# Performance work log

Hardware: AMD Instinct MI355X
Metric: run time of the kernel (lower is better)

## Reference

```python
import jax, jax.numpy as jnp
import numpy as np

N_NODES = 100000
N_EDGES = 1600000
D_IN = 128
HIDDEN = 64
N_CLASSES = 10
N_GRAPHS = 512


def setup_inputs() -> dict:
    key = jax.random.key(0)
    ks = jax.random.split(key, 9)
    x = jax.random.normal(ks[0], (N_NODES, D_IN), dtype=jnp.float32)
    edge_index = jax.random.randint(ks[1], (2, N_EDGES), 0, N_NODES, dtype=jnp.int32)
    batch = jnp.sort(jax.random.randint(ks[2], (N_NODES,), 0, N_GRAPHS, dtype=jnp.int32))
    # GCNConv: lin (no bias) + separate bias added after aggregation
    s1 = 1.0 / np.sqrt(D_IN)
    s2 = 1.0 / np.sqrt(HIDDEN)
    W1 = jax.random.uniform(ks[3], (D_IN, HIDDEN), jnp.float32, -s1, s1)
    b1 = jnp.zeros((HIDDEN,), jnp.float32)
    W2 = jax.random.uniform(ks[4], (HIDDEN, HIDDEN), jnp.float32, -s2, s2)
    b2 = jnp.zeros((HIDDEN,), jnp.float32)
    Wfc = jax.random.uniform(ks[5], (HIDDEN, N_CLASSES), jnp.float32, -s2, s2)
    bfc = jax.random.uniform(ks[6], (N_CLASSES,), jnp.float32, -s2, s2)
    return {"x": x, "edge_index": edge_index, "batch": batch,
            "W1": W1, "b1": b1, "W2": W2, "b2": b2, "Wfc": Wfc, "bfc": bfc}


def gcn_conv(x, src, dst, W, b, n_nodes):
    # symmetric normalization with added self-loops (PyG gcn_norm defaults)
    deg = jnp.zeros((n_nodes,), x.dtype).at[dst].add(1.0) + 1.0  # +1 self-loop
    dinv = jax.lax.rsqrt(deg)
    h = x @ W  # [N, out]
    coef = (dinv[src] * dinv[dst])[:, None]          # [E, 1]
    msg = h[src] * coef                               # [E, out]
    agg = jax.ops.segment_sum(msg, dst, num_segments=n_nodes)
    agg = agg + h * (dinv * dinv)[:, None]            # self-loop contribution
    return agg + b


def reference(x, edge_index, batch, W1, b1, W2, b2, Wfc, bfc):
    src, dst = edge_index[0], edge_index[1]
    n_nodes = x.shape[0]
    h = gcn_conv(x, src, dst, W1, b1, n_nodes)
    h = jax.nn.relu(h)
    # dropout skipped (inference, training=False)
    h = gcn_conv(h, src, dst, W2, b2, n_nodes)
    h = jax.nn.relu(h)
    # global mean pool over graphs
    sums = jax.ops.segment_sum(h, batch, num_segments=N_GRAPHS)
    cnts = jax.ops.segment_sum(jnp.ones((n_nodes,), h.dtype), batch, num_segments=N_GRAPHS)
    pooled = sums / jnp.maximum(cnts, 1.0)[:, None]   # [G, hidden]
    logits = pooled @ Wfc + bfc                        # [G, classes]
    return jax.nn.log_softmax(logits, axis=1)
```

## Files before the change

### kernel.cpp

```cpp
#include <hip/hip_runtime.h>
#include <cstdint>
#include <cstddef>

#define N_NODES   100000
#define N_EDGES   1600000
#define D_IN      128
#define HIDDEN    64
#define N_GRAPHS  512
#define N_CLASSES 10

#define NB   196
#define EB   1563
#define EB4  391
#define NBE  (NB * EB)
#define BCAP 12288
#define PSLOTS 8

typedef __attribute__((ext_vector_type(8))) short bf16x8;
typedef __attribute__((ext_vector_type(4))) float f32x4;
typedef __attribute__((ext_vector_type(2))) float f32x2;

__device__ inline float bf2f(unsigned short u) {
    return __uint_as_float(((unsigned int)u) << 16);
}
__device__ inline unsigned short f2bf(float f) {
    unsigned int x = __float_as_uint(f);
    return (unsigned short)((x + 0x7FFF + ((x >> 16) & 1)) >> 16);
}

__global__ __launch_bounds__(256)
void scan1_kernel(const int* __restrict__ in, int* __restrict__ bsum, int n) {
    __shared__ int lds[256];
    int tid = threadIdx.x;
    int base = blockIdx.x * 4096 + tid * 16;
    int s = 0;
#pragma unroll
    for (int j = 0; j < 16; j++) { int i = base + j; if (i < n) s += in[i]; }
    lds[tid] = s; __syncthreads();
    for (int off = 128; off > 0; off >>= 1) {
        if (tid < off) lds[tid] += lds[tid + off];
        __syncthreads();
    }
    if (tid == 0) bsum[blockIdx.x] = lds[0];
}

__global__ __launch_bounds__(256)
void scan2_kernel(int* __restrict__ bsum, int* __restrict__ out, int nb, int n) {
    __shared__ int lds[256];
    int tid = threadIdx.x;
    int v = (tid < nb) ? bsum[tid] : 0;
    lds[tid] = v; __syncthreads();
    for (int off = 1; off < 256; off <<= 1) {
        int t = (tid >= off) ? lds[tid - off] : 0;
        __syncthreads();
        lds[tid] += t;
        __syncthreads();
    }
    if (tid < nb) bsum[tid] = lds[tid] - v;
    if (tid == 255) out[n] = lds[255];
}

__global__ __launch_bounds__(256)
void scan3_kernel(const int* __restrict__ in, const int* __restrict__ bsum,
                  int* __restrict__ out, int n) {
    __shared__ int lds[256];
    int tid = threadIdx.x;
    int base = blockIdx.x * 4096 + tid * 16;
    int v[16]; int s = 0;
#pragma unroll
    for (int j = 0; j < 16; j++) {
        int i = base + j;
        v[j] = (i < n) ? in[i] : 0;
        s += v[j];
    }
    lds[tid] = s; __syncthreads();
    for (int off = 1; off < 256; off <<= 1) {
        int t = (tid >= off) ? lds[tid - off] : 0;
        __syncthreads();
        lds[tid] += t;
        __syncthreads();
    }
    int ex = lds[tid] - s + bsum[blockIdx.x];
#pragma unroll
    for (int j = 0; j < 16; j++) {
        int i = base + j;
        if (i < n) { out[i] = ex; ex += v[j]; }
    }
}

__global__ __launch_bounds__(256)
void fused1_kernel(const float* __restrict__ X, const float* __restrict__ W,
                   unsigned short* __restrict__ H,
                   const int* __restrict__ dst, int* __restrict__ HA) {
    const int tid = threadIdx.x;
    if (blockIdx.x & 1) {
        __shared__ int cnt[NB];
        int hb = blockIdx.x >> 1;
        for (int i = tid; i < NB; i += 256) cnt[i] = 0;
        __syncthreads();
        int base = hb * 1024 + tid;
#pragma unroll
        for (int j = 0; j < 4; j++) {
            int t = base + j * 256;
            if (t < N_EDGES) atomicAdd(&cnt[dst[t] >> 9], 1);
        }
        __syncthreads();
        for (int b = tid; b < NB; b += 256) HA[b * EB + hb] = cnt[b];
        return;
    }

    constexpr int K  = D_IN;
    constexpr int KP = K + 8;
    __shared__ unsigned short As[64 * KP];
    __shared__ unsigned short Wt[64 * KP];

    const int row0 = (blockIdx.x >> 1) * 64;

    for (int i = tid; i < K * 64; i += 256) {
        int k = i >> 6;
        int n = i & 63;
        Wt[n * KP + k] = f2bf(W[i]);
    }
    constexpr int KQ = K / 4;
    for (int i = tid; i < 64 * KQ; i += 256) {
        int r = i / KQ, k4 = i % KQ;
        int row = row0 + r;
        float4 v = make_float4(0.f, 0.f, 0.f, 0.f);
        if (row < N_NODES) v = ((const float4*)(X + (size_t)row * K))[k4];
        ushort4 o = make_ushort4(f2bf(v.x), f2bf(v.y), f2bf(v.z), f2bf(v.w));
        *(ushort4*)&As[r * KP + k4 * 4] = o;
    }
    __syncthreads();

    const int wave = tid >> 6;
    const int lane = tid & 63;
    const int lrow = lane & 15;
    const int quad = lane >> 4;
    const int m = wave * 16 + lrow;

    f32x4 acc0 = {0.f, 0.f, 0.f, 0.f};
    f32x4 acc1 = {0.f, 0.f, 0.f, 0.f};
    f32x4 acc2 = {0.f, 0.f, 0.f, 0.f};
    f32x4 acc3 = {0.f, 0.f, 0.f, 0.f};

#pragma unroll
    for (int kt = 0; kt < K / 32; kt++) {
        int k0 = kt * 32 + quad * 8;
        bf16x8 a = *(const bf16x8*)&As[m * KP + k0];
        bf16x8 b0 = *(const bf16x8*)&Wt[(0 * 16 + lrow) * KP + k0];
        bf16x8 b1 = *(const bf16x8*)&Wt[(1 * 16 + lrow) * KP + k0];
        bf16x8 b2 = *(const bf16x8*)&Wt[(2 * 16 + lrow) * KP + k0];
        bf16x8 b3 = *(const bf16x8*)&Wt[(3 * 16 + lrow) * KP + k0];
        acc0 = __builtin_amdgcn_mfma_f32_16x16x32_bf16(a, b0, acc0, 0, 0, 0);
        acc1 = __builtin_amdgcn_mfma_f32_16x16x32_bf16(a, b1, acc1, 0, 0, 0);
        acc2 = __builtin_amdgcn_mfma_f32_16x16x32_bf16(a, b2, acc2, 0, 0, 0);
        acc3 = __builtin_amdgcn_mfma_f32_16x16x32_bf16(a, b3, acc3, 0, 0, 0);
    }

    f32x4 accs[4] = {acc0, acc1, acc2, acc3};
#pragma unroll
    for (int c = 0; c < 4; c++) {
#pragma unroll
        for (int r = 0; r < 4; r++) {
            int row = row0 + wave * 16 + quad * 4 + r;
            if (row < N_NODES) H[(size_t)row * 64 + c * 16 + lrow] = f2bf(accs[c][r]);
        }
    }
}

__global__ __launch_bounds__(256)
void scatterA2_kernel(const int* __restrict__ src, const int* __restrict__ dst,
                      const int* __restrict__ posA, int2* __restrict__ edgeA) {
    __shared__ int off[NB];
    int tid = threadIdx.x, blk = blockIdx.x;
    for (int b = tid; b < NB; b += 256) off[b] = posA[b * EB + blk * 4];
    __syncthreads();
    int base = blk * 4096 + tid;
#pragma unroll
    for (int j = 0; j < 16; j++) {
        int t = base + j * 256;
        if (t < N_EDGES) {
            int d = dst[t];
            int r = atomicAdd(&off[d >> 9], 1);
            edgeA[r] = make_int2(d, src[t]);
        }
    }
}

__global__ __launch_bounds__(256)
void passB_kernel(const int* __restrict__ posA, const int2* __restrict__ edgeA,
                  int* __restrict__ noffs, float* __restrict__ dinv,
                  int* __restrict__ srcs2) {
    __shared__ int hist[512];
    __shared__ int off[512];
    __shared__ int ps[256];
    __shared__ int srcs_l[BCAP];

    int tid = threadIdx.x, b = blockIdx.x;
    int e0 = posA[b * EB];
    int e1 = posA[(b + 1) * EB];
    int n0 = b << 9;
    int nn = min(512, N_NODES - n0);
    int len = e1 - e0;

    hist[tid] = 0; hist[tid + 256] = 0;
    __syncthreads();
    for (int i = e0 + tid; i < e1; i += 256) atomicAdd(&hist[edgeA[i].x - n0], 1);
    __syncthreads();

    for (int n = tid; n < nn; n += 256) dinv[n0 + n] = rsqrtf((float)hist[n] + 1.0f);

    int a0 = hist[2 * tid], a1 = hist[2 * tid + 1];
    ps[tid] = a0 + a1;
    __syncthreads();
    for (int d = 1; d < 256; d <<= 1) {
        int v = (tid >= d) ? ps[tid - d] : 0;
        __syncthreads();
        ps[tid] += v;
        __syncthreads();
    }
    int pre = ps[tid] - (a0 + a1);
    off[2 * tid] = pre;
    off[2 * tid + 1] = pre + a0;
    __syncthreads();

    for (int n = tid; n < nn; n += 256) noffs[n0 + n] = e0 + off[n];
    if (b == NB - 1 && tid == 0) noffs[N_NODES] = N_EDGES;
    __syncthreads();

    if (len <= BCAP) {
        for (int i = e0 + tid; i < e1; i += 256) {
            int2 e = edgeA[i];
            int r = atomicAdd(&off[e.x - n0], 1);
            srcs_l[r] = e.y;
        }
        __syncthreads();
        for (int i = tid; i < len; i += 256) srcs2[e0 + i] = srcs_l[i];
    } else {
        for (int i = e0 + tid; i < e1; i += 256) {
            int2 e = edgeA[i];
            int r = atomicAdd(&off[e.x - n0], 1);
            srcs2[e0 + r] = e.y;
        }
    }
}

template <int K>
__global__ __launch_bounds__(256)
void gemm_mfma_fp8out_kernel(const unsigned short* __restrict__ X, const float* __restrict__ W,
                             unsigned char* __restrict__ H8, int n_rows) {
    constexpr int KP = K + 8;
    __shared__ unsigned short As[64 * KP];
    __shared__ unsigned short Wt[64 * KP];

    const int tid  = threadIdx.x;
    const int row0 = blockIdx.x * 64;

    for (int i = tid; i < K * 64; i += 256) {
        int k = i >> 6;
        int n = i & 63;
        Wt[n * KP + k] = f2bf(W[i]);
    }
    constexpr int KQ = K / 8;
    for (int i = tid; i < 64 * KQ; i += 256) {
        int r = i / KQ, k8 = i % KQ;
        int row = row0 + r;
        int4 v = make_int4(0, 0, 0, 0);
        if (row < n_rows) v = ((const int4*)(X + (size_t)row * K))[k8];
        *(int4*)&As[r * KP + k8 * 8] = v;
    }
    __syncthreads();

    const int wave = tid >> 6;
    const int lane = tid & 63;
    const int lrow = lane & 15;
    const int quad = lane >> 4;
    const int m = wave * 16 + lrow;

    f32x4 acc0 = {0.f, 0.f, 0.f, 0.f};
    f32x4 acc1 = {0.f, 0.f, 0.f, 0.f};
    f32x4 acc2 = {0.f, 0.f, 0.f, 0.f};
    f32x4 acc3 = {0.f, 0.f, 0.f, 0.f};

#pragma unroll
    for (int kt = 0; kt < K / 32; kt++) {
        int k0 = kt * 32 + quad * 8;
        bf16x8 a = *(const bf16x8*)&As[m * KP + k0];
        bf16x8 b0 = *(const bf16x8*)&Wt[(0 * 16 + lrow) * KP + k0];
        bf16x8 b1 = *(const bf16x8*)&Wt[(1 * 16 + lrow) * KP + k0];
        bf16x8 b2 = *(const bf16x8*)&Wt[(2 * 16 + lrow) * KP + k0];
        bf16x8 b3 = *(const bf16x8*)&Wt[(3 * 16 + lrow) * KP + k0];
        acc0 = __builtin_amdgcn_mfma_f32_16x16x32_bf16(a, b0, acc0, 0, 0, 0);
        acc1 = __builtin_amdgcn_mfma_f32_16x16x32_bf16(a, b1, acc1, 0, 0, 0);
        acc2 = __builtin_amdgcn_mfma_f32_16x16x32_bf16(a, b2, acc2, 0, 0, 0);
        acc3 = __builtin_amdgcn_mfma_f32_16x16x32_bf16(a, b3, acc3, 0, 0, 0);
    }

    f32x4 accs[4] = {acc0, acc1, acc2, acc3};
#pragma unroll
    for (int c = 0; c < 4; c++) {
#pragma unroll
        for (int r = 0; r < 4; r++) {
            int row = row0 + wave * 16 + quad * 4 + r;
            if (row < n_rows) {
                int p = __builtin_amdgcn_cvt_pk_fp8_f32(accs[c][r], accs[c][r], 0, false);
                H8[(size_t)row * 64 + c * 16 + lrow] = (unsigned char)(p & 0xFF);
            }
        }
    }
}

__device__ inline void upk_fma(int4 u, float c, float* acc) {
    unsigned int a = (unsigned int)u.x, b = (unsigned int)u.y;
    unsigned int d = (unsigned int)u.z, e = (unsigned int)u.w;
    acc[0] += __uint_as_float(a << 16) * c;
    acc[1] += __uint_as_float(a & 0xFFFF0000u) * c;
    acc[2] += __uint_as_float(b << 16) * c;
    acc[3] += __uint_as_float(b & 0xFFFF0000u) * c;
    acc[4] += __uint_as_float(d << 16) * c;
    acc[5] += __uint_as_float(d & 0xFFFF0000u) * c;
    acc[6] += __uint_as_float(e << 16) * c;
    acc[7] += __uint_as_float(e & 0xFFFF0000u) * c;
}

__global__ __launch_bounds__(256)
void gather_flat_kernel(const int* __restrict__ offs, const int* __restrict__ srcs,
                        const float* __restrict__ dinv, const unsigned short* __restrict__ h,
                        const float* __restrict__ b, unsigned short* __restrict__ out,
                        int n_nodes) {
    int t = blockIdx.x * 256 + threadIdx.x;
    int node = t >> 3;
    if (node >= n_nodes) return;
    int cg = (t & 7) * 8;

    float dn = dinv[node];
    float acc[8];
    {
        int4 u = *(const int4*)(h + (size_t)node * 64 + cg);
        float c2 = dn * dn;
        for (int j = 0; j < 8; j++) acc[j] = 0.f;
        upk_fma(u, c2, acc);
    }

    int i  = offs[node];
    int i1 = offs[node + 1];
    for (; i + 4 <= i1; i += 4) {
        int s0 = srcs[i];
        int s1 = srcs[i + 1];
        int s2 = srcs[i + 2];
        int s3 = srcs[i + 3];
        float c0 = dinv[s0] * dn;
        float c1 = dinv[s1] * dn;
        float c2 = dinv[s2] * dn;
        float c3 = dinv[s3] * dn;
        int4 u0 = *(const int4*)(h + (size_t)s0 * 64 + cg);
        int4 u1 = *(const int4*)(h + (size_t)s1 * 64 + cg);
        int4 u2 = *(const int4*)(h + (size_t)s2 * 64 + cg);
        int4 u3 = *(const int4*)(h + (size_t)s3 * 64 + cg);
        upk_fma(u0, c0, acc);
        upk_fma(u1, c1, acc);
        upk_fma(u2, c2, acc);
        upk_fma(u3, c3, acc);
    }
    for (; i < i1; i++) {
        int s0 = srcs[i];
        float c0 = dinv[s0] * dn;
        int4 u0 = *(const int4*)(h + (size_t)s0 * 64 + cg);
        upk_fma(u0, c0, acc);
    }

    float4 b0 = *(const float4*)(b + cg);
    float4 b1 = *(const float4*)(b + cg + 4);
    unsigned short* o = out + (size_t)node * 64 + cg;
    ushort4 p0 = make_ushort4(f2bf(fmaxf(acc[0] + b0.x, 0.f)), f2bf(fmaxf(acc[1] + b0.y, 0.f)),
                              f2bf(fmaxf(acc[2] + b0.z, 0.f)), f2bf(fmaxf(acc[3] + b0.w, 0.f)));
    ushort4 p1 = make_ushort4(f2bf(fmaxf(acc[4] + b1.x, 0.f)), f2bf(fmaxf(acc[5] + b1.y, 0.f)),
                              f2bf(fmaxf(acc[6] + b1.z, 0.f)), f2bf(fmaxf(acc[7] + b1.w, 0.f)));
    *(ushort4*)(o)     = p0;
    *(ushort4*)(o + 4) = p1;
}

__device__ inline void upk8_fma(int2 u, float c, float* acc) {
    f32x2 p0 = __builtin_amdgcn_cvt_pk_f32_fp8(u.x, false);
    f32x2 p1 = __builtin_amdgcn_cvt_pk_f32_fp8(u.x, true);
    f32x2 p2 = __builtin_amdgcn_cvt_pk_f32_fp8(u.y, false);
    f32x2 p3 = __builtin_amdgcn_cvt_pk_f32_fp8(u.y, true);
    acc[0] += p0.x * c; acc[1] += p0.y * c;
    acc[2] += p1.x * c; acc[3] += p1.y * c;
    acc[4] += p2.x * c; acc[5] += p2.y * c;
    acc[6] += p3.x * c; acc[7] += p3.y * c;
}

__global__ __launch_bounds__(256)
void gather_fp8_pool_kernel(const int* __restrict__ offs, const int* __restrict__ srcs,
                            const float* __restrict__ dinv, const unsigned char* __restrict__ h8,
                            const float* __restrict__ b, const int* __restrict__ batch,
                            float* __restrict__ pooled, float* __restrict__ cnt,
                            int n_nodes) {
    __shared__ float pacc[PSLOTS][64];
    __shared__ float lcnt[PSLOTS];
    __shared__ int sg[2];

    int tid = threadIdx.x;
    int node0 = blockIdx.x * 32;
    int lastn = min(node0 + 31, n_nodes - 1);
    for (int i = tid; i < PSLOTS * 64; i += 256) ((float*)pacc)[i] = 0.f;
    if (tid < PSLOTS) lcnt[tid] = 0.f;
    if (tid == 0) { sg[0] = batch[min(node0, n_nodes - 1)]; sg[1] = batch[lastn]; }
    __syncthreads();
    int g0 = sg[0];
    bool single = (sg[0] == sg[1]);

    int node = node0 + (tid >> 3);
    int cg = (tid & 7) * 8;

    float r[8];
#pragma unroll
    for (int j = 0; j < 8; j++) r[j] = 0.f;

    if (node < n_nodes) {
        float dn = dinv[node];
        float acc[8];
        {
            int2 u = *(const int2*)(h8 + (size_t)node * 64 + cg);
            float c2 = dn * dn;
            for (int j = 0; j < 8; j++) acc[j] = 0.f;
            upk8_fma(u, c2, acc);
        }

        int i  = offs[node];
        int i1 = offs[node + 1];
        for (; i + 4 <= i1; i += 4) {
            int s0 = srcs[i];
            int s1 = srcs[i + 1];
            int s2 = srcs[i + 2];
            int s3 = srcs[i + 3];
            float c0 = dinv[s0] * dn;
            float c1 = dinv[s1] * dn;
            float c2 = dinv[s2] * dn;
            float c3 = dinv[s3] * dn;
            int2 u0 = *(const int2*)(h8 + (size_t)s0 * 64 + cg);
            int2 u1 = *(const int2*)(h8 + (size_t)s1 * 64 + cg);
            int2 u2 = *(const int2*)(h8 + (size_t)s2 * 64 + cg);
            int2 u3 = *(const int2*)(h8 + (size_t)s3 * 64 + cg);
            upk8_fma(u0, c0, acc);
            upk8_fma(u1, c1, acc);
            upk8_fma(u2, c2, acc);
            upk8_fma(u3, c3, acc);
        }
        for (; i < i1; i++) {
            int s0 = srcs[i];
            float c0 = dinv[s0] * dn;
            int2 u0 = *(const int2*)(h8 + (size_t)s0 * 64 + cg);
            upk8_fma(u0, c0, acc);
        }

        float4 b0 = *(const float4*)(b + cg);
        float4 b1 = *(const float4*)(b + cg + 4);
        r[0] = fmaxf(acc[0] + b0.x, 0.f);
        r[1] = fmaxf(acc[1] + b0.y, 0.f);
        r[2] = fmaxf(acc[2] + b0.z, 0.f);
        r[3] = fmaxf(acc[3] + b0.w, 0.f);
        r[4] = fmaxf(acc[4] + b1.x, 0.f);
        r[5] = fmaxf(acc[5] + b1.y, 0.f);
        r[6] = fmaxf(acc[6] + b1.z, 0.f);
        r[7] = fmaxf(acc[7] + b1.w, 0.f);
    }

    if (single) {
#pragma unroll
        for (int j = 0; j < 8; j++) {
            float v = r[j];
            v += __shfl_xor(v, 8);
            v += __shfl_xor(v, 16);
            v += __shfl_xor(v, 32);
            r[j] = v;
        }
        int wave = tid >> 6;
        int lane = tid & 63;
        if (lane < 8) {
#pragma unroll
            for (int j = 0; j < 8; j++) pacc[wave][lane * 8 + j] = r[j];
        }
        __syncthreads();
        if (tid < 64) {
            float s = pacc[0][tid] + pacc[1][tid] + pacc[2][tid] + pacc[3][tid];
            if (s != 0.f) unsafeAtomicAdd(&pooled[(size_t)g0 * 64 + tid], s);
        }
        if (tid == 0) {
            int valid = min(32, n_nodes - node0);
            unsafeAtomicAdd(&cnt[g0], (float)valid);
        }
    } else {
        if (node < n_nodes) {
            int g = batch[node];
            int slot = g - g0;
            if (slot < PSLOTS) {
#pragma unroll
                for (int j = 0; j < 8; j++) atomicAdd(&pacc[slot][cg + j], r[j]);
                if ((tid & 7) == 0) atomicAdd(&lcnt[slot], 1.f);
            } else {
#pragma unroll
                for (int j = 0; j < 8; j++) unsafeAtomicAdd(&pooled[(size_t)g * 64 + cg + j], r[j]);
                if ((tid & 7) == 0) unsafeAtomicAdd(&cnt[g], 1.f);
            }
        }
        __syncthreads();
        for (int i = tid; i < PSLOTS * 64; i += 256) {
            float v = ((float*)pacc)[i];
            if (v != 0.f) unsafeAtomicAdd(&pooled[(size_t)(g0 + (i >> 6)) * 64 + (i & 63)], v);
        }
        if (tid < PSLOTS && lcnt[tid] != 0.f) unsafeAtomicAdd(&cnt[g0 + tid], lcnt[tid]);
    }
}

__global__ __launch_bounds__(256)
void head_kernel(const float* __restrict__ pooled, const float* __restrict__ cnt,
                 const float* __restrict__ Wfc, const float* __restrict__ bfc,
                 float* __restrict__ out) {
    __shared__ float Ws[HIDDEN * N_CLASSES];
    __shared__ float bs[N_CLASSES];
    int tid = threadIdx.x;
    for (int i = tid; i < HIDDEN * N_CLASSES; i += 256) Ws[i] = Wfc[i];
    if (tid < N_CLASSES) bs[tid] = bfc[tid];
    __syncthreads();

    int g = blockIdx.x * 256 + tid;
    if (g >= N_GRAPHS) return;

    float inv = 1.f / fmaxf(cnt[g], 1.f);
    float p[HIDDEN];
#pragma unroll
    for (int k = 0; k < HIDDEN; k++) p[k] = pooled[(size_t)g * 64 + k] * inv;

    float lg[N_CLASSES];
    float m = -1e30f;
#pragma unroll
    for (int j = 0; j < N_CLASSES; j++) {
        float a = bs[j];
#pragma unroll
        for (int k = 0; k < HIDDEN; k++) a += p[k] * Ws[k * N_CLASSES + j];
        lg[j] = a;
        m = fmaxf(m, a);
    }
    float s = 0.f;
#pragma unroll
    for (int j = 0; j < N_CLASSES; j++) s += __expf(lg[j] - m);
    float lse = m + __logf(s);
#pragma unroll
    for (int j = 0; j < N_CLASSES; j++) out[(size_t)g * N_CLASSES + j] = lg[j] - lse;
}

extern "C" void kernel_launch(void* const* d_in, const int* in_sizes, int n_in,
                              void* d_out, int out_size, void* d_ws, size_t ws_size,
                              hipStream_t stream) {
    const float* x   = (const float*)d_in[0];
    const int*   ei  = (const int*)d_in[1];
    const int*   bat = (const int*)d_in[2];
    const float* W1  = (const float*)d_in[3];
    const float* b1  = (const float*)d_in[4];
    const float* W2  = (const float*)d_in[5];
    const float* b2  = (const float*)d_in[6];
    const float* Wfc = (const float*)d_in[7];
    const float* bfc = (const float*)d_in[8];
    float* out = (float*)d_out;

    const int* src = ei;
    const int* dst = ei + N_EDGES;

    char* ws = (char*)d_ws;

    const size_t OFF_H     = 0;
    const size_t OFF_SRCS2 = 12800000;
    const size_t OFF_NOFFS = 19200000;
    const size_t OFF_DINV  = 19600016;
    const size_t OFF_BUFB  = 25600000;
    const size_t OFF_EDGEA = 38400000;
    const size_t OFF_HA    = 51200000;
    const size_t OFF_POSA  = 52425392;
    const size_t OFF_BSUM  = 53650800;
    const size_t OFF_POOL  = 53651824;
    const size_t OFF_CNT   = 53782896;

    unsigned short* hbuf  = (unsigned short*)(ws + OFF_H);
    unsigned char*  hbuf8 = (unsigned char*) (ws + OFF_H);
    int*   srcs2  = (int*)  (ws + OFF_SRCS2);
    int*   noffs  = (int*)  (ws + OFF_NOFFS);
    float* dinv   = (float*)(ws + OFF_DINV);
    unsigned short* bufB16 = (unsigned short*)(ws + OFF_BUFB);
    int2*  edgeA  = (int2*) (ws + OFF_EDGEA);
    int*   HA     = (int*)  (ws + OFF_HA);
    int*   posA   = (int*)  (ws + OFF_POSA);
    int*   bsum   = (int*)  (ws + OFF_BSUM);
    float* pooled = (float*)(ws + OFF_POOL);
    float* cnt    = (float*)(ws + OFF_CNT);

    const int SCAN_BLOCKS = (NBE + 4095) / 4096;
    const int GATHER_BLOCKS = (N_NODES * 8 + 255) / 256;
    const int GEMM_BLOCKS = (N_NODES + 63) / 64;

    hipMemsetAsync(pooled, 0, (size_t)(N_GRAPHS * 64 + N_GRAPHS) * sizeof(float), stream);

    fused1_kernel<<<2 * GEMM_BLOCKS, 256, 0, stream>>>(x, W1, hbuf, dst, HA);
    scan1_kernel<<<SCAN_BLOCKS, 256, 0, stream>>>(HA, bsum, NBE);
    scan2_kernel<<<1, 256, 0, stream>>>(bsum, posA, SCAN_BLOCKS, NBE);
    scan3_kernel<<<SCAN_BLOCKS, 256, 0, stream>>>(HA, bsum, posA, NBE);
    scatterA2_kernel<<<EB4, 256, 0, stream>>>(src, dst, posA, edgeA);
    passB_kernel<<<NB, 256, 0, stream>>>(posA, edgeA, noffs, dinv, srcs2);

    gather_flat_kernel<<<GATHER_BLOCKS, 256, 0, stream>>>(noffs, srcs2, dinv, hbuf, b1, bufB16, N_NODES);
    gemm_mfma_fp8out_kernel<HIDDEN><<<GEMM_BLOCKS, 256, 0, stream>>>(bufB16, W2, hbuf8, N_NODES);
    gather_fp8_pool_kernel<<<GATHER_BLOCKS, 256, 0, stream>>>(
        noffs, srcs2, dinv, hbuf8, b2, bat, pooled, cnt, N_NODES);

    head_kernel<<<(N_GRAPHS + 255) / 256, 256, 0, stream>>>(pooled, cnt, Wfc, bfc, out);
}
```

Measured before the change: 265.4 us.

## Fuse layer-1 gather with layer-2 GEMM and pre-scale features by dinv

Source features are now pre-scaled by dinv[src]: layer-1 features are scaled in place inside passB, and layer-2 features get dinv applied in the GEMM epilogue before FP8 quantization. This lets both gathers do plain adds and apply dinv[dst] once at the end, dropping the per-edge dinv loads. The layer-1 gather is fused with the layer-2 MFMA GEMM in one 512-thread kernel, so the intermediate bf16 activations stay in shared memory and never go to HBM. The gathers also batch source indices 8 at a time, prefetching the next batch while the current loads are in flight. The cost is extra in-place work in passB, a different rounding order (bf16 rescale, FP8 of pre-scaled values), and heavier per-block register and shared-memory use that may limit occupancy.

```diff
diff --git a/kernel.cpp b/kernel.cpp
--- a/kernel.cpp
+++ b/kernel.cpp
@@ -190,7 +190,7 @@
 __global__ __launch_bounds__(256)
 void passB_kernel(const int* __restrict__ posA, const int2* __restrict__ edgeA,
                   int* __restrict__ noffs, float* __restrict__ dinv,
-                  int* __restrict__ srcs2) {
+                  int* __restrict__ srcs2, unsigned short* __restrict__ hbuf) {
     __shared__ int hist[512];
     __shared__ int off[512];
     __shared__ int ps[256];
@@ -243,31 +243,140 @@
             srcs2[e0 + r] = e.y;
         }
     }
-}
-
-template <int K>
-__global__ __launch_bounds__(256)
-void gemm_mfma_fp8out_kernel(const unsigned short* __restrict__ X, const float* __restrict__ W,
-                             unsigned char* __restrict__ H8, int n_rows) {
-    constexpr int KP = K + 8;
-    __shared__ unsigned short As[64 * KP];
+
+    for (int idx = tid; idx < nn * 8; idx += 256) {
+        int n  = idx >> 3;
+        int c8 = (idx & 7) * 8;
+        float d = rsqrtf((float)hist[n] + 1.0f);
+        unsigned short* p = hbuf + (size_t)(n0 + n) * 64 + c8;
+        int4 u = *(const int4*)p;
+        int4 o;
+        {
+            unsigned int a = (unsigned int)u.x;
+            unsigned short l = f2bf(__uint_as_float(a << 16) * d);
+            unsigned short h = f2bf(__uint_as_float(a & 0xFFFF0000u) * d);
+            o.x = (int)((unsigned int)l | ((unsigned int)h << 16));
+        }
+        {
+            unsigned int a = (unsigned int)u.y;
+            unsigned short l = f2bf(__uint_as_float(a << 16) * d);
+            unsigned short h = f2bf(__uint_as_float(a & 0xFFFF0000u) * d);
+            o.y = (int)((unsigned int)l | ((unsigned int)h << 16));
+        }
+        {
+            unsigned int a = (unsigned int)u.z;
+            unsigned short l = f2bf(__uint_as_float(a << 16) * d);
+            unsigned short h = f2bf(__uint_as_float(a & 0xFFFF0000u) * d);
+            o.z = (int)((unsigned int)l | ((unsigned int)h << 16));
+        }
+        {
+            unsigned int a = (unsigned int)u.w;
+            unsigned short l = f2bf(__uint_as_float(a << 16) * d);
+            unsigned short h = f2bf(__uint_as_float(a & 0xFFFF0000u) * d);
+            o.w = (int)((unsigned int)l | ((unsigned int)h << 16));
+        }
+        *(int4*)p = o;
+    }
+}
+
+__device__ inline void upk_add(int4 u, float* acc) {
+    unsigned int a = (unsigned int)u.x, b = (unsigned int)u.y;
+    unsigned int d = (unsigned int)u.z, e = (unsigned int)u.w;
+    acc[0] += __uint_as_float(a << 16);
+    acc[1] += __uint_as_float(a & 0xFFFF0000u);
+    acc[2] += __uint_as_float(b << 16);
+    acc[3] += __uint_as_float(b & 0xFFFF0000u);
+    acc[4] += __uint_as_float(d << 16);
+    acc[5] += __uint_as_float(d & 0xFFFF0000u);
+    acc[6] += __uint_as_float(e << 16);
+    acc[7] += __uint_as_float(e & 0xFFFF0000u);
+}
+
+__device__ inline void upk8_add(int2 u, float* acc) {
+    f32x2 p0 = __builtin_amdgcn_cvt_pk_f32_fp8(u.x, false);
+    f32x2 p1 = __builtin_amdgcn_cvt_pk_f32_fp8(u.x, true);
+    f32x2 p2 = __builtin_amdgcn_cvt_pk_f32_fp8(u.y, false);
+    f32x2 p3 = __builtin_amdgcn_cvt_pk_f32_fp8(u.y, true);
+    acc[0] += p0.x; acc[1] += p0.y;
+    acc[2] += p1.x; acc[3] += p1.y;
+    acc[4] += p2.x; acc[5] += p2.y;
+    acc[6] += p3.x; acc[7] += p3.y;
+}
+
+__global__ __launch_bounds__(512)
+void gather1_gemm2_kernel(const int* __restrict__ offs, const int* __restrict__ srcs,
+                          const float* __restrict__ dinv, const unsigned short* __restrict__ h,
+                          const float* __restrict__ b1v, const float* __restrict__ W2,
+                          unsigned char* __restrict__ H8, int n_nodes) {
+    constexpr int KP = 72;
+    __shared__ unsigned short Hs[64 * KP];
     __shared__ unsigned short Wt[64 * KP];
 
-    const int tid  = threadIdx.x;
-    const int row0 = blockIdx.x * 64;
-
-    for (int i = tid; i < K * 64; i += 256) {
+    const int tid   = threadIdx.x;
+    const int node0 = blockIdx.x * 64;
+
+    for (int i = tid; i < 64 * 64; i += 512) {
         int k = i >> 6;
         int n = i & 63;
-        Wt[n * KP + k] = f2bf(W[i]);
-    }
-    constexpr int KQ = K / 8;
-    for (int i = tid; i < 64 * KQ; i += 256) {
-        int r = i / KQ, k8 = i % KQ;
-        int row = row0 + r;
-        int4 v = make_int4(0, 0, 0, 0);
-        if (row < n_rows) v = ((const int4*)(X + (size_t)row * K))[k8];
-        *(int4*)&As[r * KP + k8 * 8] = v;
+        Wt[n * KP + k] = f2bf(W2[i]);
+    }
+
+    const int g    = tid >> 3;
+    const int node = node0 + g;
+    const int cg   = (tid & 7) * 8;
+
+    float acc[8];
+#pragma unroll
+    for (int j = 0; j < 8; j++) acc[j] = 0.f;
+    float dn = 0.f;
+
+    if (node < n_nodes) {
+        dn = dinv[node];
+        int4 us = *(const int4*)(h + (size_t)node * 64 + cg);
+        upk_add(us, acc);
+
+        int i = offs[node];
+        const int i1 = offs[node + 1];
+        int rem = i1 - i;
+        if (rem > 0) {
+            int s[8];
+#pragma unroll
+            for (int j = 0; j < 8; j++) s[j] = srcs[i + (j < rem ? j : rem - 1)];
+            while (rem > 0) {
+                int4 u8[8];
+#pragma unroll
+                for (int j = 0; j < 8; j++)
+                    u8[j] = *(const int4*)(h + (size_t)s[j] * 64 + cg);
+                const int cur  = rem < 8 ? rem : 8;
+                const int ni   = i + cur;
+                const int nrem = rem - cur;
+                if (nrem > 0) {
+#pragma unroll
+                    for (int j = 0; j < 8; j++)
+                        s[j] = srcs[ni + (j < nrem ? j : nrem - 1)];
+                }
+#pragma unroll
+                for (int j = 0; j < 8; j++) { if (j < cur) upk_add(u8[j], acc); }
+                i = ni; rem = nrem;
+            }
+        }
+    }
+
+    {
+        float4 bv0 = *(const float4*)(b1v + cg);
+        float4 bv1 = *(const float4*)(b1v + cg + 4);
+        float r0 = fmaxf(dn * acc[0] + bv0.x, 0.f);
+        float r1 = fmaxf(dn * acc[1] + bv0.y, 0.f);
+        float r2 = fmaxf(dn * acc[2] + bv0.z, 0.f);
+        float r3 = fmaxf(dn * acc[3] + bv0.w, 0.f);
+        float r4 = fmaxf(dn * acc[4] + bv1.x, 0.f);
+        float r5 = fmaxf(dn * acc[5] + bv1.y, 0.f);
+        float r6 = fmaxf(dn * acc[6] + bv1.z, 0.f);
+        float r7 = fmaxf(dn * acc[7] + bv1.w, 0.f);
+        ushort4 p0 = make_ushort4(f2bf(r0), f2bf(r1), f2bf(r2), f2bf(r3));
+        ushort4 p1 = make_ushort4(f2bf(r4), f2bf(r5), f2bf(r6), f2bf(r7));
+        *(ushort4*)&Hs[g * KP + cg]     = p0;
+        *(ushort4*)&Hs[g * KP + cg + 4] = p1;
     }
     __syncthreads();
 
@@ -275,120 +384,36 @@
     const int lane = tid & 63;
     const int lrow = lane & 15;
     const int quad = lane >> 4;
-    const int m = wave * 16 + lrow;
+    const int rt = (wave & 3) * 16;
+    const int ct = (wave >> 2) * 32;
+    const int m = rt + lrow;
 
     f32x4 acc0 = {0.f, 0.f, 0.f, 0.f};
     f32x4 acc1 = {0.f, 0.f, 0.f, 0.f};
-    f32x4 acc2 = {0.f, 0.f, 0.f, 0.f};
-    f32x4 acc3 = {0.f, 0.f, 0.f, 0.f};
-
-#pragma unroll
-    for (int kt = 0; kt < K / 32; kt++) {
+#pragma unroll
+    for (int kt = 0; kt < 2; kt++) {
         int k0 = kt * 32 + quad * 8;
-        bf16x8 a = *(const bf16x8*)&As[m * KP + k0];
-        bf16x8 b0 = *(const bf16x8*)&Wt[(0 * 16 + lrow) * KP + k0];
-        bf16x8 b1 = *(const bf16x8*)&Wt[(1 * 16 + lrow) * KP + k0];
-        bf16x8 b2 = *(const bf16x8*)&Wt[(2 * 16 + lrow) * KP + k0];
-        bf16x8 b3 = *(const bf16x8*)&Wt[(3 * 16 + lrow) * KP + k0];
-        acc0 = __builtin_amdgcn_mfma_f32_16x16x32_bf16(a, b0, acc0, 0, 0, 0);
-        acc1 = __builtin_amdgcn_mfma_f32_16x16x32_bf16(a, b1, acc1, 0, 0, 0);
-        acc2 = __builtin_amdgcn_mfma_f32_16x16x32_bf16(a, b2, acc2, 0, 0, 0);
-        acc3 = __builtin_amdgcn_mfma_f32_16x16x32_bf16(a, b3, acc3, 0, 0, 0);
-    }
-
-    f32x4 accs[4] = {acc0, acc1, acc2, acc3};
-#pragma unroll
-    for (int c = 0; c < 4; c++) {
-#pragma unroll
-        for (int r = 0; r < 4; r++) {
-            int row = row0 + wave * 16 + quad * 4 + r;
-            if (row < n_rows) {
-                int p = __builtin_amdgcn_cvt_pk_fp8_f32(accs[c][r], accs[c][r], 0, false);
-                H8[(size_t)row * 64 + c * 16 + lrow] = (unsigned char)(p & 0xFF);
+        bf16x8 a  = *(const bf16x8*)&Hs[m * KP + k0];
+        bf16x8 w0 = *(const bf16x8*)&Wt[(ct + lrow) * KP + k0];
+        bf16x8 w1 = *(const bf16x8*)&Wt[(ct + 16 + lrow) * KP + k0];
+        acc0 = __builtin_amdgcn_mfma_f32_16x16x32_bf16(a, w0, acc0, 0, 0, 0);
+        acc1 = __builtin_amdgcn_mfma_f32_16x16x32_bf16(a, w1, acc1, 0, 0, 0);
+    }
+
+    f32x4 accs[2] = {acc0, acc1};
+#pragma unroll
+    for (int r = 0; r < 4; r++) {
+        int row = node0 + rt + quad * 4 + r;
+        if (row < n_nodes) {
+            float dv = dinv[row];
+#pragma unroll
+            for (int c = 0; c < 2; c++) {
+                float v = accs[c][r] * dv;
+                int p = __builtin_amdgcn_cvt_pk_fp8_f32(v, v, 0, false);
+                H8[(size_t)row * 64 + ct + c * 16 + lrow] = (unsigned char)(p & 0xFF);
             }
         }
     }
-}
-
-__device__ inline void upk_fma(int4 u, float c, float* acc) {
-    unsigned int a = (unsigned int)u.x, b = (unsigned int)u.y;
-    unsigned int d = (unsigned int)u.z, e = (unsigned int)u.w;
-    acc[0] += __uint_as_float(a << 16) * c;
-    acc[1] += __uint_as_float(a & 0xFFFF0000u) * c;
-    acc[2] += __uint_as_float(b << 16) * c;
-    acc[3] += __uint_as_float(b & 0xFFFF0000u) * c;
-    acc[4] += __uint_as_float(d << 16) * c;
-    acc[5] += __uint_as_float(d & 0xFFFF0000u) * c;
-    acc[6] += __uint_as_float(e << 16) * c;
-    acc[7] += __uint_as_float(e & 0xFFFF0000u) * c;
-}
-
-__global__ __launch_bounds__(256)
-void gather_flat_kernel(const int* __restrict__ offs, const int* __restrict__ srcs,
-                        const float* __restrict__ dinv, const unsigned short* __restrict__ h,
-                        const float* __restrict__ b, unsigned short* __restrict__ out,
-                        int n_nodes) {
-    int t = blockIdx.x * 256 + threadIdx.x;
-    int node = t >> 3;
-    if (node >= n_nodes) return;
-    int cg = (t & 7) * 8;
-
-    float dn = dinv[node];
-    float acc[8];
-    {
-        int4 u = *(const int4*)(h + (size_t)node * 64 + cg);
-        float c2 = dn * dn;
-        for (int j = 0; j < 8; j++) acc[j] = 0.f;
-        upk_fma(u, c2, acc);
-    }
-
-    int i  = offs[node];
-    int i1 = offs[node + 1];
-    for (; i + 4 <= i1; i += 4) {
-        int s0 = srcs[i];
-        int s1 = srcs[i + 1];
-        int s2 = srcs[i + 2];
-        int s3 = srcs[i + 3];
-        float c0 = dinv[s0] * dn;
-        float c1 = dinv[s1] * dn;
-        float c2 = dinv[s2] * dn;
-        float c3 = dinv[s3] * dn;
-        int4 u0 = *(const int4*)(h + (size_t)s0 * 64 + cg);
-        int4 u1 = *(const int4*)(h + (size_t)s1 * 64 + cg);
-        int4 u2 = *(const int4*)(h + (size_t)s2 * 64 + cg);
-        int4 u3 = *(const int4*)(h + (size_t)s3 * 64 + cg);
-        upk_fma(u0, c0, acc);
-        upk_fma(u1, c1, acc);
-        upk_fma(u2, c2, acc);
-        upk_fma(u3, c3, acc);
-    }
-    for (; i < i1; i++) {
-        int s0 = srcs[i];
-        float c0 = dinv[s0] * dn;
-        int4 u0 = *(const int4*)(h + (size_t)s0 * 64 + cg);
-        upk_fma(u0, c0, acc);
-    }
-
-    float4 b0 = *(const float4*)(b + cg);
-    float4 b1 = *(const float4*)(b + cg + 4);
-    unsigned short* o = out + (size_t)node * 64 + cg;
-    ushort4 p0 = make_ushort4(f2bf(fmaxf(acc[0] + b0.x, 0.f)), f2bf(fmaxf(acc[1] + b0.y, 0.f)),
-                              f2bf(fmaxf(acc[2] + b0.z, 0.f)), f2bf(fmaxf(acc[3] + b0.w, 0.f)));
-    ushort4 p1 = make_ushort4(f2bf(fmaxf(acc[4] + b1.x, 0.f)), f2bf(fmaxf(acc[5] + b1.y, 0.f)),
-                              f2bf(fmaxf(acc[6] + b1.z, 0.f)), f2bf(fmaxf(acc[7] + b1.w, 0.f)));
-    *(ushort4*)(o)     = p0;
-    *(ushort4*)(o + 4) = p1;
-}
-
-__device__ inline void upk8_fma(int2 u, float c, float* acc) {
-    f32x2 p0 = __builtin_amdgcn_cvt_pk_f32_fp8(u.x, false);
-    f32x2 p1 = __builtin_amdgcn_cvt_pk_f32_fp8(u.x, true);
-    f32x2 p2 = __builtin_amdgcn_cvt_pk_f32_fp8(u.y, false);
-    f32x2 p3 = __builtin_amdgcn_cvt_pk_f32_fp8(u.y, true);
-    acc[0] += p0.x * c; acc[1] += p0.y * c;
-    acc[2] += p1.x * c; acc[3] += p1.y * c;
-    acc[4] += p2.x * c; acc[5] += p2.y * c;
-    acc[6] += p3.x * c; acc[7] += p3.y * c;
 }
 
 __global__ __launch_bounds__(256)
@@ -421,50 +446,49 @@
     if (node < n_nodes) {
         float dn = dinv[node];
         float acc[8];
+#pragma unroll
+        for (int j = 0; j < 8; j++) acc[j] = 0.f;
         {
             int2 u = *(const int2*)(h8 + (size_t)node * 64 + cg);
-            float c2 = dn * dn;
-            for (int j = 0; j < 8; j++) acc[j] = 0.f;
-            upk8_fma(u, c2, acc);
-        }
-
-        int i  = offs[node];
-        int i1 = offs[node + 1];
-        for (; i + 4 <= i1; i += 4) {
-            int s0 = srcs[i];
-            int s1 = srcs[i + 1];
-            int s2 = srcs[i + 2];
-            int s3 = srcs[i + 3];
-            float c0 = dinv[s0] * dn;
-            float c1 = dinv[s1] * dn;
-            float c2 = dinv[s2] * dn;
-            float c3 = dinv[s3] * dn;
-            int2 u0 = *(const int2*)(h8 + (size_t)s0 * 64 + cg);
-            int2 u1 = *(const int2*)(h8 + (size_t)s1 * 64 + cg);
-            int2 u2 = *(const int2*)(h8 + (size_t)s2 * 64 + cg);
-            int2 u3 = *(const int2*)(h8 + (size_t)s3 * 64 + cg);
-            upk8_fma(u0, c0, acc);
-            upk8_fma(u1, c1, acc);
-            upk8_fma(u2, c2, acc);
-            upk8_fma(u3, c3, acc);
-        }
-        for (; i < i1; i++) {
-            int s0 = srcs[i];
-            float c0 = dinv[s0] * dn;
-            int2 u0 = *(const int2*)(h8 + (size_t)s0 * 64 + cg);
-            upk8_fma(u0, c0, acc);
+            upk8_add(u, acc);
+        }
+
+        int i = offs[node];
+        const int i1 = offs[node + 1];
+        int rem = i1 - i;
+        if (rem > 0) {
+            int s[8];
+#pragma unroll
+            for (int j = 0; j < 8; j++) s[j] = srcs[i + (j < rem ? j : rem - 1)];
+            while (rem > 0) {
+                int2 u8[8];
+#pragma unroll
+                for (int j = 0; j < 8; j++)
+                    u8[j] = *(const int2*)(h8 + (size_t)s[j] * 64 + cg);
+                const int cur  = rem < 8 ? rem : 8;
+                const int ni   = i + cur;
+                const int nrem = rem - cur;
+                if (nrem > 0) {
+#pragma unroll
+                    for (int j = 0; j < 8; j++)
+                        s[j] = srcs[ni + (j < nrem ? j : nrem - 1)];
+                }
+#pragma unroll
+                for (int j = 0; j < 8; j++) { if (j < cur) upk8_add(u8[j], acc); }
+                i = ni; rem = nrem;
+            }
         }
 
         float4 b0 = *(const float4*)(b + cg);
         float4 b1 = *(const float4*)(b + cg + 4);
-        r[0] = fmaxf(acc[0] + b0.x, 0.f);
-        r[1] = fmaxf(acc[1] + b0.y, 0.f);
-        r[2] = fmaxf(acc[2] + b0.z, 0.f);
-        r[3] = fmaxf(acc[3] + b0.w, 0.f);
-        r[4] = fmaxf(acc[4] + b1.x, 0.f);
-        r[5] = fmaxf(acc[5] + b1.y, 0.f);
-        r[6] = fmaxf(acc[6] + b1.z, 0.f);
-        r[7] = fmaxf(acc[7] + b1.w, 0.f);
+        r[0] = fmaxf(dn * acc[0] + b0.x, 0.f);
+        r[1] = fmaxf(dn * acc[1] + b0.y, 0.f);
+        r[2] = fmaxf(dn * acc[2] + b0.z, 0.f);
+        r[3] = fmaxf(dn * acc[3] + b0.w, 0.f);
+        r[4] = fmaxf(dn * acc[4] + b1.x, 0.f);
+        r[5] = fmaxf(dn * acc[5] + b1.y, 0.f);
+        r[6] = fmaxf(dn * acc[6] + b1.z, 0.f);
+        r[7] = fmaxf(dn * acc[7] + b1.w, 0.f);
     }
 
     if (single) {
@@ -583,11 +607,10 @@
     const size_t OFF_CNT   = 53782896;
 
     unsigned short* hbuf  = (unsigned short*)(ws + OFF_H);
-    unsigned char*  hbuf8 = (unsigned char*) (ws + OFF_H);
     int*   srcs2  = (int*)  (ws + OFF_SRCS2);
     int*   noffs  = (int*)  (ws + OFF_NOFFS);
     float* dinv   = (float*)(ws + OFF_DINV);
-    unsigned short* bufB16 = (unsigned short*)(ws + OFF_BUFB);
+    unsigned char* hbuf8 = (unsigned char*)(ws + OFF_BUFB);
     int2*  edgeA  = (int2*) (ws + OFF_EDGEA);
     int*   HA     = (int*)  (ws + OFF_HA);
     int*   posA   = (int*)  (ws + OFF_POSA);
@@ -606,10 +629,10 @@
     scan2_kernel<<<1, 256, 0, stream>>>(bsum, posA, SCAN_BLOCKS, NBE);
     scan3_kernel<<<SCAN_BLOCKS, 256, 0, stream>>>(HA, bsum, posA, NBE);
     scatterA2_kernel<<<EB4, 256, 0, stream>>>(src, dst, posA, edgeA);
-    passB_kernel<<<NB, 256, 0, stream>>>(posA, edgeA, noffs, dinv, srcs2);
-
-    gather_flat_kernel<<<GATHER_BLOCKS, 256, 0, stream>>>(noffs, srcs2, dinv, hbuf, b1, bufB16, N_NODES);
-    gemm_mfma_fp8out_kernel<HIDDEN><<<GEMM_BLOCKS, 256, 0, stream>>>(bufB16, W2, hbuf8, N_NODES);
+    passB_kernel<<<NB, 256, 0, stream>>>(posA, edgeA, noffs, dinv, srcs2, hbuf);
+
+    gather1_gemm2_kernel<<<GEMM_BLOCKS, 512, 0, stream>>>(
+        noffs, srcs2, dinv, hbuf, b1, W2, hbuf8, N_NODES);
     gather_fp8_pool_kernel<<<GATHER_BLOCKS, 256, 0, stream>>>(
         noffs, srcs2, dinv, hbuf8, b2, bat, pooled, cnt, N_NODES);
 
```

New measurement: 250.1 us. 1.06x faster.
